# Performance work log

Measured on AMD Instinct MI355X. Metric: run time of the kernel, lower is better.

The kernel has to match this reference:

```python
import jax, jax.numpy as jnp
import numpy as np

B, S, D = 8, 4096, 256


def setup_inputs() -> dict:
    key = jax.random.key(0)
    kq, kk, kv, kb = jax.random.split(key, 4)
    q = jax.random.normal(kq, (B, S, D), dtype=jnp.float32)
    k = jax.random.normal(kk, (B, S, D), dtype=jnp.float32)
    v = jax.random.normal(kv, (B, S, D), dtype=jnp.float32)
    beta = jax.random.uniform(kb, (B, S), dtype=jnp.float32)
    return {"q": q, "k": k, "v": v, "beta": beta}


def reference(q, k, v, beta):
    # Delta-rule linear attention recurrence:
    #   h_t = beta_t * h_{t-1} + k_t^T v_t   (h: [B, D, D])
    #   o_t = q_t @ h_t                      (o: [B, D])
    dtype = q.dtype
    b, s, d = q.shape
    h0 = jnp.zeros((b, d, d), dtype=dtype)

    def step(h, inp):
        q_t, k_t, v_t, b_t = inp  # q_t/k_t/v_t: [B, D], b_t: [B]
        h = h * b_t[:, None, None] + jnp.einsum('bi,bj->bij', k_t, v_t)
        o_t = jnp.einsum('bi,bij->bj', q_t, h)
        return h, o_t

    xs = (q.transpose(1, 0, 2), k.transpose(1, 0, 2),
          v.transpose(1, 0, 2), beta.T)  # time-major
    _, out = jax.lax.scan(step, h0, xs)  # out: [S, B, D]
    return out.transpose(1, 0, 2)  # [B, S, D]
```

## Files before the change

kernel.cpp:

```cpp
#include <hip/hip_runtime.h>
#include <math.h>


#define B_ 8
#define S_ 4096
#define D_ 256
#define L_ 64
#define C_ (S_ / L_)
#define BC_ (B_ * C_)

typedef __attribute__((ext_vector_type(8))) short s8v;
typedef __attribute__((ext_vector_type(4))) float f4v;
typedef unsigned short u16;
typedef unsigned int u32;

__device__ __forceinline__ u16 f2bf(float f) {
  u32 u = __float_as_uint(f);
  u += 0x7FFF + ((u >> 16) & 1);
  return (u16)(u >> 16);
}
__device__ __forceinline__ s8v pack8(float4 a, float4 b) {
  s8v r;
  r[0] = (short)f2bf(a.x); r[1] = (short)f2bf(a.y);
  r[2] = (short)f2bf(a.z); r[3] = (short)f2bf(a.w);
  r[4] = (short)f2bf(b.x); r[5] = (short)f2bf(b.y);
  r[6] = (short)f2bf(b.z); r[7] = (short)f2bf(b.w);
  return r;
}

__global__ __launch_bounds__(512, 4) void ks_summary3(
    const float* __restrict__ kg, const float* __restrict__ vg,
    const float* __restrict__ beta, u16* __restrict__ A,
    float* __restrict__ P)
{
  __shared__ float ls[L_];
  __shared__ __align__(16) u16 KT[D_][72];
  __shared__ __align__(16) u16 VT[D_][72];

  const int bc = blockIdx.x;
  const int b = bc / C_, c = bc % C_;
  const int tid = threadIdx.x;
  const float* betap = beta + (size_t)b * S_ + (size_t)c * L_;
  const float* kbase = kg + ((size_t)b * S_ + (size_t)c * L_) * D_;
  const float* vbase = vg + ((size_t)b * S_ + (size_t)c * L_) * D_;

  if (tid < 64) {
    float x = log2f(fmaxf(betap[tid], 1e-30f));
#pragma unroll
    for (int off = 1; off < 64; off <<= 1) {
      float y = __shfl_up(x, off);
      if (tid >= off) x += y;
    }
    ls[tid] = x;
    if (tid == 63) P[bc] = exp2f(x);
  }
  __syncthreads();
  const float ltot = ls[63];

  {
    const int half = tid >> 8;
    const int t2 = tid & 255;
    const int iL = t2 & 7;
    const int s0 = (t2 >> 3) * 2;
    const float* src0 = (half == 0 ? kbase : vbase) + (size_t)s0 * D_;
    const float* src1 = src0 + D_;
    float w0 = 1.f, w1 = 1.f;
    if (half == 0) { w0 = exp2f(ltot - ls[s0]); w1 = exp2f(ltot - ls[s0 + 1]); }
    u16 (*dst)[72] = (half == 0) ? KT : VT;
#pragma unroll
    for (int p = 0; p < 8; ++p) {
      const int i0 = p * 32 + iL * 4;
      float a0[4], a1[4];
      *(float4*)a0 = *(const float4*)(src0 + i0);
      *(float4*)a1 = *(const float4*)(src1 + i0);
#pragma unroll
      for (int u = 0; u < 4; ++u)
        *(u32*)&dst[i0 + u][s0] =
            (u32)f2bf(a0[u] * w0) | ((u32)f2bf(a1[u] * w1) << 16);
    }
  }
  __syncthreads();

  const int lane = tid & 63, wave = tid >> 6;
  const int quad = lane >> 4, l15 = lane & 15;
  const int m0 = wave * 32;
  u16* Ab = A + (size_t)bc * D_ * D_;

  for (int ng = 0; ng < 4; ++ng) {
    f4v acc[2][4];
#pragma unroll
    for (int mt = 0; mt < 2; ++mt)
#pragma unroll
      for (int nt = 0; nt < 4; ++nt) acc[mt][nt] = (f4v){0.f, 0.f, 0.f, 0.f};

#pragma unroll
    for (int ks = 0; ks < 2; ++ks) {
      const int so = ks * 32 + quad * 8;
      s8v av[2], bv[4];
#pragma unroll
      for (int mt = 0; mt < 2; ++mt)
        av[mt] = *(const s8v*)&VT[m0 + mt * 16 + l15][so];
#pragma unroll
      for (int nt = 0; nt < 4; ++nt)
        bv[nt] = *(const s8v*)&KT[ng * 64 + nt * 16 + l15][so];
#pragma unroll
      for (int mt = 0; mt < 2; ++mt)
#pragma unroll
        for (int nt = 0; nt < 4; ++nt)
          acc[mt][nt] = __builtin_amdgcn_mfma_f32_16x16x32_bf16(
              av[mt], bv[nt], acc[mt][nt], 0, 0, 0);
    }
#pragma unroll
    for (int mt = 0; mt < 2; ++mt)
#pragma unroll
      for (int r = 0; r < 4; ++r) {
        const int j = m0 + mt * 16 + quad * 4 + r;
#pragma unroll
        for (int nt = 0; nt < 4; ++nt) {
          const int i = ng * 64 + nt * 16 + l15;
          const float v = acc[mt][nt][r];
          const float o = __shfl_xor(v, 1);
          if (!(lane & 1)) {
            *(u32*)(Ab + (size_t)j * D_ + i) =
                (u32)f2bf(v) | ((u32)f2bf(o) << 16);
          }
        }
      }
  }
}

__global__ __launch_bounds__(256) void ks_scan3(
    u16* __restrict__ A, const float* __restrict__ P)
{
  const int g = blockIdx.x;
  const int b = g >> 7;
  const int idx = ((g & 127) << 8) + threadIdx.x;
  u16* base = A + (size_t)b * ((size_t)C_ * D_ * D_) + (size_t)idx * 2;
  const float* Pb = P + b * C_;

  float h0 = 0.f, h1 = 0.f;
  u32 nxt = *(const u32*)base;
  float pn = Pb[0];
#pragma unroll 4
  for (int c = 0; c < C_; ++c) {
    const u32 u = nxt;
    const float pc = pn;
    u16* p = base + (size_t)c * (D_ * D_);
    if (c + 1 < C_) {
      nxt = *(const u32*)(p + (size_t)(D_ * D_));
      pn = Pb[c + 1];
    }
    const float a0 = __uint_as_float(u << 16);
    const float a1 = __uint_as_float(u & 0xFFFF0000u);
    *(u32*)p = (u32)f2bf(h0) | ((u32)f2bf(h1) << 16);
    h0 = fmaf(pc, h0, a0);
    h1 = fmaf(pc, h1, a1);
  }
}

__global__ __launch_bounds__(512, 4) void ks_output3(
    const float* __restrict__ qg, const float* __restrict__ kg,
    const float* __restrict__ vg, const float* __restrict__ beta,
    const u16* __restrict__ Hg, float* __restrict__ outg)
{
  __shared__ float ls[L_];
  __shared__ float cv[L_];
  __shared__ __align__(16) u16 QB[L_][264];
  __shared__ __align__(16) u16 UN[D_ * 72];
  __shared__ __align__(16) u16 Tm[L_][72];
  u16 (*KB)[264] = (u16(*)[264])UN;
  u16 (*VT)[72] = (u16(*)[72])UN;

  const int bc = blockIdx.x;
  const int b = bc / C_, c = bc % C_;
  const int tid = threadIdx.x;
  const float* betap = beta + (size_t)b * S_ + (size_t)c * L_;
  const float* qbase = qg + ((size_t)b * S_ + (size_t)c * L_) * D_;
  const float* kbase = kg + ((size_t)b * S_ + (size_t)c * L_) * D_;
  const float* vbase = vg + ((size_t)b * S_ + (size_t)c * L_) * D_;
  const u16* Hb = Hg + (size_t)bc * D_ * D_;

  if (tid < 64) {
    float x = log2f(fmaxf(betap[tid], 1e-30f));
#pragma unroll
    for (int off = 1; off < 64; off <<= 1) {
      float y = __shfl_up(x, off);
      if (tid >= off) x += y;
    }
    ls[tid] = x;
  }

  {
    const int half = tid >> 8;
    const int t2 = tid & 255;
    const int t = t2 >> 2;
    const int cg = (t2 & 3) * 8;
    const float* src = (half == 0 ? qbase : kbase) + (size_t)t * D_ + cg;
    u16 (*dst)[264] = (half == 0) ? QB : KB;
#pragma unroll
    for (int p = 0; p < 8; ++p) {
      const int c0 = cg + p * 32;
      const s8v pk =
          pack8(*(const float4*)(src + p * 32), *(const float4*)(src + p * 32 + 4));
      *(s8v*)&dst[t][c0] = pk;
    }
  }
  __syncthreads();
  if (tid < 64) cv[tid] = exp2f(ls[tid]);

  const int lane = tid & 63, wave = tid >> 6;
  const int quad = lane >> 4, l15 = lane & 15;

  {
    const int mA = (wave & 3) * 16;
    const int nB = (wave >> 2) * 2;
    f4v accA[2];
#pragma unroll
    for (int i = 0; i < 2; ++i) accA[i] = (f4v){0.f, 0.f, 0.f, 0.f};
#pragma unroll
    for (int kd = 0; kd < 8; ++kd) {
      const int d0 = kd * 32 + quad * 8;
      const s8v af = *(const s8v*)&QB[mA + l15][d0];
#pragma unroll
      for (int i = 0; i < 2; ++i) {
        const s8v bf = *(const s8v*)&KB[(nB + i) * 16 + l15][d0];
        accA[i] = __builtin_amdgcn_mfma_f32_16x16x32_bf16(af, bf, accA[i],
                                                          0, 0, 0);
      }
    }
#pragma unroll
    for (int i = 0; i < 2; ++i)
#pragma unroll
      for (int r = 0; r < 4; ++r) {
        const int t = mA + quad * 4 + r;
        const int s = (nB + i) * 16 + l15;
        const float m = (s <= t) ? exp2f(ls[t] - ls[s]) : 0.f;
        Tm[t][s] = f2bf(accA[i][r] * m);
      }
  }
  __syncthreads();

  {
    const int iL = tid & 15;
    const int s0 = (tid >> 4) * 2;
#pragma unroll
    for (int p = 0; p < 4; ++p) {
      const int i0 = p * 64 + iL * 4;
      float a0[4], a1[4];
      *(float4*)a0 = *(const float4*)(vbase + (size_t)s0 * D_ + i0);
      *(float4*)a1 = *(const float4*)(vbase + (size_t)(s0 + 1) * D_ + i0);
#pragma unroll
      for (int u = 0; u < 4; ++u)
        *(u32*)&VT[i0 + u][s0] = (u32)f2bf(a0[u]) | ((u32)f2bf(a1[u]) << 16);
    }
  }
  __syncthreads();

  const int j0w = wave * 32;
  f4v accS[4][2], accH[4][2];
#pragma unroll
  for (int mt = 0; mt < 4; ++mt)
#pragma unroll
    for (int nt = 0; nt < 2; ++nt) {
      accS[mt][nt] = (f4v){0.f, 0.f, 0.f, 0.f};
      accH[mt][nt] = (f4v){0.f, 0.f, 0.f, 0.f};
    }

#pragma unroll
  for (int ks = 0; ks < 2; ++ks) {
    const int so = ks * 32 + quad * 8;
    s8v af[4], bf[2];
#pragma unroll
    for (int mt = 0; mt < 4; ++mt)
      af[mt] = *(const s8v*)&Tm[mt * 16 + l15][so];
#pragma unroll
    for (int nt = 0; nt < 2; ++nt)
      bf[nt] = *(const s8v*)&VT[j0w + nt * 16 + l15][so];
#pragma unroll
    for (int mt = 0; mt < 4; ++mt)
#pragma unroll
      for (int nt = 0; nt < 2; ++nt)
        accS[mt][nt] = __builtin_amdgcn_mfma_f32_16x16x32_bf16(
            af[mt], bf[nt], accS[mt][nt], 0, 0, 0);
  }

#pragma unroll
  for (int ks = 0; ks < 8; ++ks) {
    const int io = ks * 32 + quad * 8;
    s8v af[4], bf[2];
#pragma unroll
    for (int mt = 0; mt < 4; ++mt)
      af[mt] = *(const s8v*)&QB[mt * 16 + l15][io];
#pragma unroll
    for (int nt = 0; nt < 2; ++nt)
      bf[nt] = *(const s8v*)(Hb + (size_t)(j0w + nt * 16 + l15) * D_ + io);
#pragma unroll
    for (int mt = 0; mt < 4; ++mt)
#pragma unroll
      for (int nt = 0; nt < 2; ++nt)
        accH[mt][nt] = __builtin_amdgcn_mfma_f32_16x16x32_bf16(
            af[mt], bf[nt], accH[mt][nt], 0, 0, 0);
  }

  float* ob = outg + ((size_t)b * S_ + (size_t)c * L_) * D_;
#pragma unroll
  for (int mt = 0; mt < 4; ++mt)
#pragma unroll
    for (int r = 0; r < 4; ++r) {
      const int t = mt * 16 + quad * 4 + r;
      const float ct = cv[t];
#pragma unroll
      for (int nt = 0; nt < 2; ++nt) {
        const int j = j0w + nt * 16 + l15;
        ob[(size_t)t * D_ + j] = accS[mt][nt][r] + ct * accH[mt][nt][r];
      }
    }
}

extern "C" void kernel_launch(void* const* d_in, const int* in_sizes, int n_in,
                              void* d_out, int out_size, void* d_ws,
                              size_t ws_size, hipStream_t stream) {
  const float* q = (const float*)d_in[0];
  const float* k = (const float*)d_in[1];
  const float* v = (const float*)d_in[2];
  const float* beta = (const float*)d_in[3];
  float* out = (float*)d_out;

  u16* A = (u16*)d_ws;
  float* P = (float*)((char*)d_ws + (size_t)BC_ * D_ * D_ * sizeof(u16));

  ks_summary3<<<dim3(BC_), dim3(512), 0, stream>>>(k, v, beta, A, P);
  ks_scan3<<<dim3(1024), dim3(256), 0, stream>>>(A, P);
  ks_output3<<<dim3(BC_), dim3(512), 0, stream>>>(q, k, v, beta, A, out);
}
```

Baseline: 186.7 us.

## Vectorize bf16 packing and stores, stage summary output via LDS, deepen scan prefetch

Replaces the manual float-to-bf16 rounding with packed hardware conversion intrinsics. The summary kernel keeps K fragments in registers, reuses the KT buffer to transpose results, and writes full 16-byte rows to global memory instead of shuffled 4-byte stores. The scan kernel prefetches two chunks ahead, and the output kernel swaps MFMA operand roles so it can emit float4 stores. LDS padding changes to a stride of 66. The extra barriers and the odd padding may add stalls or bank conflicts.

```diff
diff --git a/kernel.cpp b/kernel.cpp
--- a/kernel.cpp
+++ b/kernel.cpp
@@ -1,4 +1,5 @@
 #include <hip/hip_runtime.h>
+#include <hip/hip_bf16.h>
 #include <math.h>
 
 
@@ -8,34 +9,33 @@
 #define L_ 64
 #define C_ (S_ / L_)
 #define BC_ (B_ * C_)
+#define STK 66
 
 typedef __attribute__((ext_vector_type(8))) short s8v;
 typedef __attribute__((ext_vector_type(4))) float f4v;
 typedef unsigned short u16;
 typedef unsigned int u32;
 
-__device__ __forceinline__ u16 f2bf(float f) {
-  u32 u = __float_as_uint(f);
-  u += 0x7FFF + ((u >> 16) & 1);
-  return (u16)(u >> 16);
-}
-__device__ __forceinline__ s8v pack8(float4 a, float4 b) {
-  s8v r;
-  r[0] = (short)f2bf(a.x); r[1] = (short)f2bf(a.y);
-  r[2] = (short)f2bf(a.z); r[3] = (short)f2bf(a.w);
-  r[4] = (short)f2bf(b.x); r[5] = (short)f2bf(b.y);
-  r[6] = (short)f2bf(b.z); r[7] = (short)f2bf(b.w);
-  return r;
-}
-
-__global__ __launch_bounds__(512, 4) void ks_summary3(
+__device__ __forceinline__ u32 pk2(float lo, float hi) {
+  union { __hip_bfloat162 h; u32 u; } cv;
+  cv.h = __float22bfloat162_rn(make_float2(lo, hi));
+  return cv.u;
+}
+__device__ __forceinline__ s8v pack8(const float4 a, const float4 b) {
+  union { u32 u[4]; s8v v; } r;
+  r.u[0] = pk2(a.x, a.y); r.u[1] = pk2(a.z, a.w);
+  r.u[2] = pk2(b.x, b.y); r.u[3] = pk2(b.z, b.w);
+  return r.v;
+}
+
+__global__ __launch_bounds__(512, 4) void ks_summary4(
     const float* __restrict__ kg, const float* __restrict__ vg,
     const float* __restrict__ beta, u16* __restrict__ A,
     float* __restrict__ P)
 {
   __shared__ float ls[L_];
-  __shared__ __align__(16) u16 KT[D_][72];
-  __shared__ __align__(16) u16 VT[D_][72];
+  __shared__ __align__(16) u16 KT[D_ * STK];
+  __shared__ __align__(16) u16 VT[D_ * STK];
 
   const int bc = blockIdx.x;
   const int b = bc / C_, c = bc % C_;
@@ -66,7 +66,7 @@
     const float* src1 = src0 + D_;
     float w0 = 1.f, w1 = 1.f;
     if (half == 0) { w0 = exp2f(ltot - ls[s0]); w1 = exp2f(ltot - ls[s0 + 1]); }
-    u16 (*dst)[72] = (half == 0) ? KT : VT;
+    u16* dst = (half == 0) ? KT : VT;
 #pragma unroll
     for (int p = 0; p < 8; ++p) {
       const int i0 = p * 32 + iL * 4;
@@ -75,16 +75,26 @@
       *(float4*)a1 = *(const float4*)(src1 + i0);
 #pragma unroll
       for (int u = 0; u < 4; ++u)
-        *(u32*)&dst[i0 + u][s0] =
-            (u32)f2bf(a0[u] * w0) | ((u32)f2bf(a1[u] * w1) << 16);
+        *(u32*)&dst[(i0 + u) * STK + s0] = pk2(a0[u] * w0, a1[u] * w1);
     }
   }
   __syncthreads();
 
   const int lane = tid & 63, wave = tid >> 6;
   const int quad = lane >> 4, l15 = lane & 15;
-  const int m0 = wave * 32;
+  const int i0w = wave * 32;
+
+  s8v af[2][2];
+#pragma unroll
+  for (int mt = 0; mt < 2; ++mt)
+#pragma unroll
+    for (int ks = 0; ks < 2; ++ks)
+      af[mt][ks] = *(const s8v*)&KT[(i0w + mt * 16 + l15) * STK +
+                                    ks * 32 + quad * 8];
+  __syncthreads();
+
   u16* Ab = A + (size_t)bc * D_ * D_;
+  u16* BN = KT;
 
   for (int ng = 0; ng < 4; ++ng) {
     f4v acc[2][4];
@@ -96,40 +106,43 @@
 #pragma unroll
     for (int ks = 0; ks < 2; ++ks) {
       const int so = ks * 32 + quad * 8;
-      s8v av[2], bv[4];
-#pragma unroll
-      for (int mt = 0; mt < 2; ++mt)
-        av[mt] = *(const s8v*)&VT[m0 + mt * 16 + l15][so];
+      s8v bv[4];
 #pragma unroll
       for (int nt = 0; nt < 4; ++nt)
-        bv[nt] = *(const s8v*)&KT[ng * 64 + nt * 16 + l15][so];
+        bv[nt] = *(const s8v*)&VT[(ng * 64 + nt * 16 + l15) * STK + so];
 #pragma unroll
       for (int mt = 0; mt < 2; ++mt)
 #pragma unroll
         for (int nt = 0; nt < 4; ++nt)
           acc[mt][nt] = __builtin_amdgcn_mfma_f32_16x16x32_bf16(
-              av[mt], bv[nt], acc[mt][nt], 0, 0, 0);
-    }
-#pragma unroll
-    for (int mt = 0; mt < 2; ++mt)
-#pragma unroll
-      for (int r = 0; r < 4; ++r) {
-        const int j = m0 + mt * 16 + quad * 4 + r;
-#pragma unroll
-        for (int nt = 0; nt < 4; ++nt) {
-          const int i = ng * 64 + nt * 16 + l15;
-          const float v = acc[mt][nt][r];
-          const float o = __shfl_xor(v, 1);
-          if (!(lane & 1)) {
-            *(u32*)(Ab + (size_t)j * D_ + i) =
-                (u32)f2bf(v) | ((u32)f2bf(o) << 16);
-          }
-        }
+              af[mt][ks], bv[nt], acc[mt][nt], 0, 0, 0);
+    }
+#pragma unroll
+    for (int mt = 0; mt < 2; ++mt)
+#pragma unroll
+      for (int nt = 0; nt < 4; ++nt) {
+        const int jl = nt * 16 + l15;
+        uint2 w;
+        w.x = pk2(acc[mt][nt][0], acc[mt][nt][1]);
+        w.y = pk2(acc[mt][nt][2], acc[mt][nt][3]);
+        *(uint2*)&BN[jl * 264 + i0w + mt * 16 + quad * 4] = w;
       }
-  }
-}
-
-__global__ __launch_bounds__(256) void ks_scan3(
+    __syncthreads();
+    {
+      const int jl = tid >> 3;
+      const int il = (tid & 7) * 8;
+#pragma unroll
+      for (int p = 0; p < 4; ++p) {
+        const int iu = il + p * 64;
+        *(s8v*)&Ab[(size_t)(ng * 64 + jl) * D_ + iu] =
+            *(const s8v*)&BN[jl * 264 + iu];
+      }
+    }
+    __syncthreads();
+  }
+}
+
+__global__ __launch_bounds__(256) void ks_scan4(
     u16* __restrict__ A, const float* __restrict__ P)
 {
   const int g = blockIdx.x;
@@ -139,37 +152,36 @@
   const float* Pb = P + b * C_;
 
   float h0 = 0.f, h1 = 0.f;
-  u32 nxt = *(const u32*)base;
-  float pn = Pb[0];
+  u32 cur = *(const u32*)base;
+  u32 nx = *(const u32*)(base + (size_t)(D_ * D_));
+  float pc = Pb[0], pn = Pb[1];
 #pragma unroll 4
   for (int c = 0; c < C_; ++c) {
-    const u32 u = nxt;
-    const float pc = pn;
     u16* p = base + (size_t)c * (D_ * D_);
-    if (c + 1 < C_) {
-      nxt = *(const u32*)(p + (size_t)(D_ * D_));
-      pn = Pb[c + 1];
-    }
-    const float a0 = __uint_as_float(u << 16);
-    const float a1 = __uint_as_float(u & 0xFFFF0000u);
-    *(u32*)p = (u32)f2bf(h0) | ((u32)f2bf(h1) << 16);
+    u32 n2 = 0; float p2 = 0.f;
+    if (c + 2 < C_) {
+      n2 = *(const u32*)(p + 2 * (size_t)(D_ * D_));
+      p2 = Pb[c + 2];
+    }
+    const float a0 = __uint_as_float(cur << 16);
+    const float a1 = __uint_as_float(cur & 0xFFFF0000u);
+    *(u32*)p = pk2(h0, h1);
     h0 = fmaf(pc, h0, a0);
     h1 = fmaf(pc, h1, a1);
-  }
-}
-
-__global__ __launch_bounds__(512, 4) void ks_output3(
+    cur = nx; pc = pn; nx = n2; pn = p2;
+  }
+}
+
+__global__ __launch_bounds__(512, 4) void ks_output4(
     const float* __restrict__ qg, const float* __restrict__ kg,
     const float* __restrict__ vg, const float* __restrict__ beta,
     const u16* __restrict__ Hg, float* __restrict__ outg)
 {
   __shared__ float ls[L_];
   __shared__ float cv[L_];
-  __shared__ __align__(16) u16 QB[L_][264];
-  __shared__ __align__(16) u16 UN[D_ * 72];
-  __shared__ __align__(16) u16 Tm[L_][72];
-  u16 (*KB)[264] = (u16(*)[264])UN;
-  u16 (*VT)[72] = (u16(*)[72])UN;
+  __shared__ __align__(16) u16 QB[L_ * 264];
+  __shared__ __align__(16) u16 UN[L_ * 264];
+  __shared__ __align__(16) u16 Tm[L_ * 72];
 
   const int bc = blockIdx.x;
   const int b = bc / C_, c = bc % C_;
@@ -196,13 +208,12 @@
     const int t = t2 >> 2;
     const int cg = (t2 & 3) * 8;
     const float* src = (half == 0 ? qbase : kbase) + (size_t)t * D_ + cg;
-    u16 (*dst)[264] = (half == 0) ? QB : KB;
+    u16* dst = (half == 0) ? QB : UN;
 #pragma unroll
     for (int p = 0; p < 8; ++p) {
-      const int c0 = cg + p * 32;
-      const s8v pk =
-          pack8(*(const float4*)(src + p * 32), *(const float4*)(src + p * 32 + 4));
-      *(s8v*)&dst[t][c0] = pk;
+      const s8v pk = pack8(*(const float4*)(src + p * 32),
+                           *(const float4*)(src + p * 32 + 4));
+      *(s8v*)&dst[t * 264 + cg + p * 32] = pk;
     }
   }
   __syncthreads();
@@ -213,33 +224,41 @@
 
   {
     const int mA = (wave & 3) * 16;
-    const int nB = (wave >> 2) * 2;
+    const int nB = (wave >> 2) * 32;
     f4v accA[2];
 #pragma unroll
     for (int i = 0; i < 2; ++i) accA[i] = (f4v){0.f, 0.f, 0.f, 0.f};
 #pragma unroll
     for (int kd = 0; kd < 8; ++kd) {
       const int d0 = kd * 32 + quad * 8;
-      const s8v af = *(const s8v*)&QB[mA + l15][d0];
+      const s8v af = *(const s8v*)&UN[(mA + l15) * 264 + d0];
 #pragma unroll
       for (int i = 0; i < 2; ++i) {
-        const s8v bf = *(const s8v*)&KB[(nB + i) * 16 + l15][d0];
+        const s8v bf = *(const s8v*)&QB[(nB + i * 16 + l15) * 264 + d0];
         accA[i] = __builtin_amdgcn_mfma_f32_16x16x32_bf16(af, bf, accA[i],
                                                           0, 0, 0);
       }
     }
 #pragma unroll
-    for (int i = 0; i < 2; ++i)
+    for (int i = 0; i < 2; ++i) {
+      const int t = nB + i * 16 + l15;
+      const float lt = ls[t];
+      const int s0 = mA + quad * 4;
+      float v[4];
 #pragma unroll
       for (int r = 0; r < 4; ++r) {
-        const int t = mA + quad * 4 + r;
-        const int s = (nB + i) * 16 + l15;
-        const float m = (s <= t) ? exp2f(ls[t] - ls[s]) : 0.f;
-        Tm[t][s] = f2bf(accA[i][r] * m);
+        const int s = s0 + r;
+        v[r] = (s <= t) ? accA[i][r] * exp2f(lt - ls[s]) : 0.f;
       }
-  }
-  __syncthreads();
-
+      uint2 w;
+      w.x = pk2(v[0], v[1]);
+      w.y = pk2(v[2], v[3]);
+      *(uint2*)&Tm[t * 72 + s0] = w;
+    }
+  }
+  __syncthreads();
+
+  u16* VT = UN;
   {
     const int iL = tid & 15;
     const int s0 = (tid >> 4) * 2;
@@ -251,17 +270,17 @@
       *(float4*)a1 = *(const float4*)(vbase + (size_t)(s0 + 1) * D_ + i0);
 #pragma unroll
       for (int u = 0; u < 4; ++u)
-        *(u32*)&VT[i0 + u][s0] = (u32)f2bf(a0[u]) | ((u32)f2bf(a1[u]) << 16);
+        *(u32*)&VT[(i0 + u) * STK + s0] = pk2(a0[u], a1[u]);
     }
   }
   __syncthreads();
 
   const int j0w = wave * 32;
-  f4v accS[4][2], accH[4][2];
-#pragma unroll
-  for (int mt = 0; mt < 4; ++mt)
-#pragma unroll
-    for (int nt = 0; nt < 2; ++nt) {
+  f4v accS[2][4], accH[2][4];
+#pragma unroll
+  for (int mt = 0; mt < 2; ++mt)
+#pragma unroll
+    for (int nt = 0; nt < 4; ++nt) {
       accS[mt][nt] = (f4v){0.f, 0.f, 0.f, 0.f};
       accH[mt][nt] = (f4v){0.f, 0.f, 0.f, 0.f};
     }
@@ -269,17 +288,17 @@
 #pragma unroll
   for (int ks = 0; ks < 2; ++ks) {
     const int so = ks * 32 + quad * 8;
-    s8v af[4], bf[2];
-#pragma unroll
-    for (int mt = 0; mt < 4; ++mt)
-      af[mt] = *(const s8v*)&Tm[mt * 16 + l15][so];
-#pragma unroll
-    for (int nt = 0; nt < 2; ++nt)
-      bf[nt] = *(const s8v*)&VT[j0w + nt * 16 + l15][so];
-#pragma unroll
-    for (int mt = 0; mt < 4; ++mt)
-#pragma unroll
-      for (int nt = 0; nt < 2; ++nt)
+    s8v af[2], bf[4];
+#pragma unroll
+    for (int mt = 0; mt < 2; ++mt)
+      af[mt] = *(const s8v*)&VT[(j0w + mt * 16 + l15) * STK + so];
+#pragma unroll
+    for (int nt = 0; nt < 4; ++nt)
+      bf[nt] = *(const s8v*)&Tm[(nt * 16 + l15) * 72 + so];
+#pragma unroll
+    for (int mt = 0; mt < 2; ++mt)
+#pragma unroll
+      for (int nt = 0; nt < 4; ++nt)
         accS[mt][nt] = __builtin_amdgcn_mfma_f32_16x16x32_bf16(
             af[mt], bf[nt], accS[mt][nt], 0, 0, 0);
   }
@@ -287,33 +306,35 @@
 #pragma unroll
   for (int ks = 0; ks < 8; ++ks) {
     const int io = ks * 32 + quad * 8;
-    s8v af[4], bf[2];
-#pragma unroll
-    for (int mt = 0; mt < 4; ++mt)
-      af[mt] = *(const s8v*)&QB[mt * 16 + l15][io];
-#pragma unroll
-    for (int nt = 0; nt < 2; ++nt)
-      bf[nt] = *(const s8v*)(Hb + (size_t)(j0w + nt * 16 + l15) * D_ + io);
-#pragma unroll
-    for (int mt = 0; mt < 4; ++mt)
-#pragma unroll
-      for (int nt = 0; nt < 2; ++nt)
+    s8v af[2], bf[4];
+#pragma unroll
+    for (int mt = 0; mt < 2; ++mt)
+      af[mt] = *(const s8v*)(Hb + (size_t)(j0w + mt * 16 + l15) * D_ + io);
+#pragma unroll
+    for (int nt = 0; nt < 4; ++nt)
+      bf[nt] = *(const s8v*)&QB[(nt * 16 + l15) * 264 + io];
+#pragma unroll
+    for (int mt = 0; mt < 2; ++mt)
+#pragma unroll
+      for (int nt = 0; nt < 4; ++nt)
         accH[mt][nt] = __builtin_amdgcn_mfma_f32_16x16x32_bf16(
             af[mt], bf[nt], accH[mt][nt], 0, 0, 0);
   }
 
   float* ob = outg + ((size_t)b * S_ + (size_t)c * L_) * D_;
 #pragma unroll
-  for (int mt = 0; mt < 4; ++mt)
-#pragma unroll
-    for (int r = 0; r < 4; ++r) {
-      const int t = mt * 16 + quad * 4 + r;
+  for (int mt = 0; mt < 2; ++mt)
+#pragma unroll
+    for (int nt = 0; nt < 4; ++nt) {
+      const int t = nt * 16 + l15;
       const float ct = cv[t];
-#pragma unroll
-      for (int nt = 0; nt < 2; ++nt) {
-        const int j = j0w + nt * 16 + l15;
-        ob[(size_t)t * D_ + j] = accS[mt][nt][r] + ct * accH[mt][nt][r];
-      }
+      const int j0 = j0w + mt * 16 + quad * 4;
+      float4 o;
+      o.x = accS[mt][nt][0] + ct * accH[mt][nt][0];
+      o.y = accS[mt][nt][1] + ct * accH[mt][nt][1];
+      o.z = accS[mt][nt][2] + ct * accH[mt][nt][2];
+      o.w = accS[mt][nt][3] + ct * accH[mt][nt][3];
+      *(float4*)(ob + (size_t)t * D_ + j0) = o;
     }
 }
 
@@ -329,7 +350,7 @@
   u16* A = (u16*)d_ws;
   float* P = (float*)((char*)d_ws + (size_t)BC_ * D_ * D_ * sizeof(u16));
 
-  ks_summary3<<<dim3(BC_), dim3(512), 0, stream>>>(k, v, beta, A, P);
-  ks_scan3<<<dim3(1024), dim3(256), 0, stream>>>(A, P);
-  ks_output3<<<dim3(BC_), dim3(512), 0, stream>>>(q, k, v, beta, A, out);
-}
+  ks_summary4<<<dim3(BC_), dim3(512), 0, stream>>>(k, v, beta, A, P);
+  ks_scan4<<<dim3(1024), dim3(256), 0, stream>>>(A, P);
+  ks_output4<<<dim3(BC_), dim3(512), 0, stream>>>(q, k, v, beta, A, out);
+}
```

Result: no change. 189.7 us (+1.6%).
